# Kernel optimization log

Hardware: AMD Instinct MI355X
Metric: run time of the kernel (lower is better)

The kernel has to match this reference:

```python
import jax, jax.numpy as jnp
import numpy as np

B, S, D_IN, D_OUT = 4, 2048, 4096, 4096
QMAX = 16  # 2**bits

def setup_inputs() -> dict:
    key = jax.random.key(0)
    k1, k2, k3, k4, k5 = jax.random.split(key, 5)
    x = jax.random.normal(k1, (B, S, D_IN), dtype=jnp.float32)
    weight_q = jax.random.randint(k2, (D_OUT, D_IN), 0, QMAX, dtype=jnp.int32)
    scale = jax.random.uniform(k3, (), dtype=jnp.float32) * 0.01 + 1e-4
    zero_point = jax.random.uniform(k4, (), dtype=jnp.float32) * QMAX
    bias = jax.random.normal(k5, (D_OUT,), dtype=jnp.float32)
    return {"x": x, "weight_q": weight_q, "scale": scale,
            "zero_point": zero_point, "bias": bias}

def reference(x, weight_q, scale, zero_point, bias):
    # Dequantize: w = (q - zero_point) * scale, then y = x @ w.T + b
    w = (weight_q.astype(jnp.float32) - zero_point) * scale  # [out, in]
    return jnp.einsum('bsi,oi->bso', x, w) + bias
```

## Files before the change

### kernel.cpp

```cpp
#include <hip/hip_runtime.h>
#include <cstdint>

#define M_DIM 8192
#define N_DIM 4096
#define K_DIM 4096
#define NT    32

typedef int i32x4 __attribute__((ext_vector_type(4)));

__device__ __forceinline__ void gload_lds16(const void* g, void* l) {
  __builtin_amdgcn_global_load_lds(
      (const __attribute__((address_space(1))) unsigned int*)(uintptr_t)g,
      (__attribute__((address_space(3))) unsigned int*)(uintptr_t)l,
      16, 0, 0);
}

__global__ __launch_bounds__(256) void prep_kernel(
    const float* __restrict__ x, const int* __restrict__ q,
    signed char* __restrict__ xq, signed char* __restrict__ wq8,
    float* __restrict__ sx, float* __restrict__ si) {
  const int tid  = threadIdx.x;
  const int lane = tid & 63;
  const int wv   = tid >> 6;
  if (blockIdx.x < 2048) {
    const int row = blockIdx.x * 4 + wv;
    const float* xr = x + (size_t)row * K_DIM;
    signed char* xo = xq + (size_t)row * K_DIM;
    float4 v[16];
    float amax = 0.f;
#pragma unroll
    for (int j = 0; j < 16; ++j) {
      v[j] = *(const float4*)(xr + j * 256 + lane * 4);
      amax = fmaxf(amax, fmaxf(fmaxf(fabsf(v[j].x), fabsf(v[j].y)),
                               fmaxf(fabsf(v[j].z), fabsf(v[j].w))));
    }
#pragma unroll
    for (int off = 32; off > 0; off >>= 1)
      amax = fmaxf(amax, __shfl_xor(amax, off, 64));
    const float inv = amax > 0.f ? 127.f / amax : 0.f;
    int isum = 0;
#pragma unroll
    for (int j = 0; j < 16; ++j) {
      int ix = __float2int_rn(v[j].x * inv);
      int iy = __float2int_rn(v[j].y * inv);
      int iz = __float2int_rn(v[j].z * inv);
      int iw = __float2int_rn(v[j].w * inv);
      isum += ix + iy + iz + iw;
      char4 o; o.x = (char)ix; o.y = (char)iy; o.z = (char)iz; o.w = (char)iw;
      *(char4*)(xo + j * 256 + lane * 4) = o;
    }
#pragma unroll
    for (int off = 32; off > 0; off >>= 1)
      isum += __shfl_xor(isum, off, 64);
    if (lane == 0) {
      sx[row] = amax * (1.f / 127.f);
      si[row] = (float)isum;
    }
  } else {
    const int bid = blockIdx.x - 2048;
    const size_t total  = (size_t)N_DIM * K_DIM;
    const size_t stride = (size_t)1024 * 4096;
    for (size_t base = (size_t)bid * 4096; base < total; base += stride) {
#pragma unroll
      for (int u = 0; u < 4; ++u) {
        const size_t idx = base + (size_t)u * 1024 + tid * 4;
        int4 w = *(const int4*)(q + idx);
        char4 o; o.x = (char)w.x; o.y = (char)w.y; o.z = (char)w.z; o.w = (char)w.w;
        *(char4*)(wq8 + idx) = o;
      }
    }
  }
}

__global__ __launch_bounds__(512) void qlinear_gemm_kernel(
    const signed char* __restrict__ A,
    const signed char* __restrict__ Bm,
    const float* __restrict__ sx,
    const float* __restrict__ si,
    const float* __restrict__ scale_p, const float* __restrict__ zp_p,
    const float* __restrict__ bias,
    float* __restrict__ out) {
  __shared__ signed char sA[2][2][16384];
  __shared__ signed char sB[2][2][16384];

  const int tid  = threadIdx.x;
  const int lane = tid & 63;
  const int w    = tid >> 6;
  const int wr   = w >> 2;
  const int wc   = w & 3;
  const int lr   = lane & 15;
  const int quad = lane >> 4;

  const int bm = blockIdx.y * 256;
  const int bn = blockIdx.x * 256;

  const int srow = lane >> 3;
  const int cg   = (lane & 7) ^ srow;
  const signed char* aG = A  + (size_t)(bm + w * 8 + srow) * K_DIM + cg * 16;
  const signed char* bG = Bm + (size_t)(bn + w * 8 + srow) * K_DIM + cg * 16;
  const int dwoff = w * 1024;

#define STG_A(dst, h, c, t) \
  gload_lds16(aG + (size_t)((h) * 128 + (c) * 64) * K_DIM + (size_t)(t) * 128, \
              (dst) + (h) * 16384 + (c) * 8192 + dwoff)
#define STG_B(dst, h, c, t) \
  gload_lds16(bG + (size_t)((h) * 128 + (c) * 64) * K_DIM + (size_t)(t) * 128, \
              (dst) + (h) * 16384 + (c) * 8192 + dwoff)

  int off[2];
#pragma unroll
  for (int ks = 0; ks < 2; ++ks)
    off[ks] = lr * 128 + (((ks * 4 + quad) ^ (lr & 7)) * 16);

  i32x4 acc[8][4] = {};
  i32x4 afr[4][2];
  i32x4 bfr[2][2][2];

  {
    signed char* dA = &sA[0][0][0];
    signed char* dB = &sB[0][0][0];
    STG_B(dB, 0, 0, 0); STG_B(dB, 0, 1, 0);
    STG_B(dB, 1, 0, 0); STG_B(dB, 1, 1, 0);
    STG_A(dA, 0, 0, 0); STG_A(dA, 1, 0, 0);
    STG_A(dA, 0, 1, 0); STG_A(dA, 1, 1, 0);
  }

  for (int t = 0; t < NT; ++t) {
    const int buf = t & 1;
    const signed char* pA = &sA[buf][wr][0];
    const signed char* pB = &sB[buf][wc >> 1][0] + (wc & 1) * 8192;
    signed char* nA = &sA[buf ^ 1][0][0];
    signed char* nB = &sB[buf ^ 1][0][0];
    const bool st = (t + 1) < NT;
    const int tn = t + 1;

    asm volatile("s_waitcnt vmcnt(2)" ::: "memory");
    if (st) { STG_B(nB, 0, 0, tn); STG_B(nB, 0, 1, tn); }
    __builtin_amdgcn_s_barrier();
#pragma unroll
    for (int m = 0; m < 4; ++m)
#pragma unroll
      for (int ks = 0; ks < 2; ++ks)
        afr[m][ks] = *(const i32x4*)(pA + m * 2048 + off[ks]);
#pragma unroll
    for (int n = 0; n < 2; ++n)
#pragma unroll
      for (int ks = 0; ks < 2; ++ks)
        bfr[0][n][ks] = *(const i32x4*)(pB + n * 2048 + off[ks]);
    __builtin_amdgcn_s_setprio(1);
#pragma unroll
    for (int m = 0; m < 4; ++m)
#pragma unroll
      for (int n = 0; n < 2; ++n)
#pragma unroll
        for (int ks = 0; ks < 2; ++ks)
          acc[m][n] = __builtin_amdgcn_mfma_i32_16x16x64_i8(
              afr[m][ks], bfr[0][n][ks], acc[m][n], 0, 0, 0);
    __builtin_amdgcn_s_setprio(0);

    if (st) { STG_B(nB, 1, 0, tn); STG_B(nB, 1, 1, tn); }
    __builtin_amdgcn_s_barrier();
#pragma unroll
    for (int n = 0; n < 2; ++n)
#pragma unroll
      for (int ks = 0; ks < 2; ++ks)
        bfr[1][n][ks] = *(const i32x4*)(pB + 4096 + n * 2048 + off[ks]);
    __builtin_amdgcn_s_setprio(1);
#pragma unroll
    for (int m = 0; m < 4; ++m)
#pragma unroll
      for (int n = 0; n < 2; ++n)
#pragma unroll
        for (int ks = 0; ks < 2; ++ks)
          acc[m][2 + n] = __builtin_amdgcn_mfma_i32_16x16x64_i8(
              afr[m][ks], bfr[1][n][ks], acc[m][2 + n], 0, 0, 0);
    __builtin_amdgcn_s_setprio(0);

    if (st) asm volatile("s_waitcnt vmcnt(4)" ::: "memory");
    else    asm volatile("s_waitcnt vmcnt(0)" ::: "memory");
    if (st) { STG_A(nA, 0, 0, tn); STG_A(nA, 1, 0, tn); }
    __builtin_amdgcn_s_barrier();
#pragma unroll
    for (int m = 0; m < 4; ++m)
#pragma unroll
      for (int ks = 0; ks < 2; ++ks)
        afr[m][ks] = *(const i32x4*)(pA + 8192 + m * 2048 + off[ks]);
    __builtin_amdgcn_s_setprio(1);
#pragma unroll
    for (int m = 0; m < 4; ++m)
#pragma unroll
      for (int n = 0; n < 2; ++n)
#pragma unroll
        for (int ks = 0; ks < 2; ++ks)
          acc[4 + m][n] = __builtin_amdgcn_mfma_i32_16x16x64_i8(
              afr[m][ks], bfr[0][n][ks], acc[4 + m][n], 0, 0, 0);
    __builtin_amdgcn_s_setprio(0);

    if (st) { STG_A(nA, 0, 1, tn); STG_A(nA, 1, 1, tn); }
    __builtin_amdgcn_s_barrier();
    __builtin_amdgcn_s_setprio(1);
#pragma unroll
    for (int m = 0; m < 4; ++m)
#pragma unroll
      for (int n = 0; n < 2; ++n)
#pragma unroll
        for (int ks = 0; ks < 2; ++ks)
          acc[4 + m][2 + n] = __builtin_amdgcn_mfma_i32_16x16x64_i8(
              afr[m][ks], bfr[1][n][ks], acc[4 + m][2 + n], 0, 0, 0);
    __builtin_amdgcn_s_setprio(0);
  }
#undef STG_A
#undef STG_B

  const float scale = *scale_p;
  const float zp    = *zp_p;
#pragma unroll
  for (int i = 0; i < 8; ++i) {
    const int gm0 = bm + wr * 128 + i * 16 + quad * 4;
    float am[4], cm[4];
#pragma unroll
    for (int r = 0; r < 4; ++r) {
      am[r] = scale * sx[gm0 + r];
      cm[r] = -am[r] * zp * si[gm0 + r];
    }
#pragma unroll
    for (int j = 0; j < 4; ++j) {
      const int gn = bn + wc * 64 + j * 16 + lr;
      const float bb = bias[gn];
#pragma unroll
      for (int r = 0; r < 4; ++r)
        out[(size_t)(gm0 + r) * N_DIM + gn] =
            am[r] * (float)acc[i][j][r] + cm[r] + bb;
    }
  }
}

extern "C" void kernel_launch(void* const* d_in, const int* in_sizes, int n_in,
                              void* d_out, int out_size, void* d_ws, size_t ws_size,
                              hipStream_t stream) {
  const float* x     = (const float*)d_in[0];
  const int*   wq    = (const int*)d_in[1];
  const float* scale = (const float*)d_in[2];
  const float* zp    = (const float*)d_in[3];
  const float* bias  = (const float*)d_in[4];
  float* out = (float*)d_out;

  signed char* xq  = (signed char*)d_ws;
  signed char* wq8 = xq + (size_t)M_DIM * K_DIM;
  float* sx = (float*)(wq8 + (size_t)N_DIM * K_DIM);
  float* si = sx + M_DIM;

  prep_kernel<<<3072, 256, 0, stream>>>(x, wq, xq, wq8, sx, si);
  dim3 grid(N_DIM / 256, M_DIM / 256);
  qlinear_gemm_kernel<<<grid, 512, 0, stream>>>(xq, wq8, sx, si, scale, zp, bias, out);
}
```

Before: 385.7 us.

## Remap GEMM blocks by XCD and restructure the K-loop with fewer barriers

Launches a 1D grid and remaps block IDs so consecutive blocks on each XCD (bid&7) cover a contiguous group of output tiles, aiming for better L2 reuse of the A and B panels. The main loop drops from four barriers to two per K step: all four B loads, then all four A loads, are issued together. Fragment LDS reads are split by k-slice, with partial lgkmcnt waits so the first k-half's MFMAs can start while the second half's reads are still in flight. This raises B-fragment register use and relies on hand-placed waitcnt and sched_barrier ordering being correct.

```diff
diff --git a/kernel.cpp b/kernel.cpp
--- a/kernel.cpp
+++ b/kernel.cpp
@@ -91,8 +91,10 @@
   const int lr   = lane & 15;
   const int quad = lane >> 4;
 
-  const int bm = blockIdx.y * 256;
-  const int bn = blockIdx.x * 256;
+  const int bid = blockIdx.x;
+  const int swz = (bid & 7) * 64 + (bid >> 3);
+  const int bm  = (swz >> 4) * 256;
+  const int bn  = (swz & 15) * 256;
 
   const int srow = lane >> 3;
   const int cg   = (lane & 7) ^ srow;
@@ -114,7 +116,7 @@
 
   i32x4 acc[8][4] = {};
   i32x4 afr[4][2];
-  i32x4 bfr[2][2][2];
+  i32x4 bfr[4][2];
 
   {
     signed char* dA = &sA[0][0][0];
@@ -135,78 +137,76 @@
     const int tn = t + 1;
 
     asm volatile("s_waitcnt vmcnt(2)" ::: "memory");
-    if (st) { STG_B(nB, 0, 0, tn); STG_B(nB, 0, 1, tn); }
     __builtin_amdgcn_s_barrier();
-#pragma unroll
-    for (int m = 0; m < 4; ++m)
-#pragma unroll
-      for (int ks = 0; ks < 2; ++ks)
-        afr[m][ks] = *(const i32x4*)(pA + m * 2048 + off[ks]);
-#pragma unroll
-    for (int n = 0; n < 2; ++n)
-#pragma unroll
-      for (int ks = 0; ks < 2; ++ks)
-        bfr[0][n][ks] = *(const i32x4*)(pB + n * 2048 + off[ks]);
-    __builtin_amdgcn_s_setprio(1);
-#pragma unroll
-    for (int m = 0; m < 4; ++m)
-#pragma unroll
-      for (int n = 0; n < 2; ++n)
-#pragma unroll
-        for (int ks = 0; ks < 2; ++ks)
-          acc[m][n] = __builtin_amdgcn_mfma_i32_16x16x64_i8(
-              afr[m][ks], bfr[0][n][ks], acc[m][n], 0, 0, 0);
-    __builtin_amdgcn_s_setprio(0);
-
-    if (st) { STG_B(nB, 1, 0, tn); STG_B(nB, 1, 1, tn); }
-    __builtin_amdgcn_s_barrier();
-#pragma unroll
-    for (int n = 0; n < 2; ++n)
-#pragma unroll
-      for (int ks = 0; ks < 2; ++ks)
-        bfr[1][n][ks] = *(const i32x4*)(pB + 4096 + n * 2048 + off[ks]);
-    __builtin_amdgcn_s_setprio(1);
-#pragma unroll
-    for (int m = 0; m < 4; ++m)
-#pragma unroll
-      for (int n = 0; n < 2; ++n)
-#pragma unroll
-        for (int ks = 0; ks < 2; ++ks)
-          acc[m][2 + n] = __builtin_amdgcn_mfma_i32_16x16x64_i8(
-              afr[m][ks], bfr[1][n][ks], acc[m][2 + n], 0, 0, 0);
+    if (st) { STG_B(nB, 0, 0, tn); STG_B(nB, 0, 1, tn);
+              STG_B(nB, 1, 0, tn); STG_B(nB, 1, 1, tn); }
+#pragma unroll
+    for (int m = 0; m < 4; ++m)
+      afr[m][0] = *(const i32x4*)(pA + m * 2048 + off[0]);
+#pragma unroll
+    for (int n = 0; n < 4; ++n)
+      bfr[n][0] = *(const i32x4*)(pB + n * 2048 + off[0]);
+    __builtin_amdgcn_sched_barrier(0);
+#pragma unroll
+    for (int m = 0; m < 4; ++m)
+      afr[m][1] = *(const i32x4*)(pA + m * 2048 + off[1]);
+#pragma unroll
+    for (int n = 0; n < 4; ++n)
+      bfr[n][1] = *(const i32x4*)(pB + n * 2048 + off[1]);
+    __builtin_amdgcn_sched_barrier(0);
+    asm volatile("s_waitcnt lgkmcnt(8)" ::: "memory");
+    __builtin_amdgcn_sched_barrier(0);
+    __builtin_amdgcn_s_setprio(1);
+#pragma unroll
+    for (int m = 0; m < 4; ++m)
+#pragma unroll
+      for (int n = 0; n < 4; ++n)
+        acc[m][n] = __builtin_amdgcn_mfma_i32_16x16x64_i8(
+            afr[m][0], bfr[n][0], acc[m][n], 0, 0, 0);
+    __builtin_amdgcn_s_setprio(0);
+    asm volatile("s_waitcnt lgkmcnt(0)" ::: "memory");
+    __builtin_amdgcn_sched_barrier(0);
+    __builtin_amdgcn_s_setprio(1);
+#pragma unroll
+    for (int m = 0; m < 4; ++m)
+#pragma unroll
+      for (int n = 0; n < 4; ++n)
+        acc[m][n] = __builtin_amdgcn_mfma_i32_16x16x64_i8(
+            afr[m][1], bfr[n][1], acc[m][n], 0, 0, 0);
     __builtin_amdgcn_s_setprio(0);
 
     if (st) asm volatile("s_waitcnt vmcnt(4)" ::: "memory");
     else    asm volatile("s_waitcnt vmcnt(0)" ::: "memory");
-    if (st) { STG_A(nA, 0, 0, tn); STG_A(nA, 1, 0, tn); }
     __builtin_amdgcn_s_barrier();
-#pragma unroll
-    for (int m = 0; m < 4; ++m)
-#pragma unroll
-      for (int ks = 0; ks < 2; ++ks)
-        afr[m][ks] = *(const i32x4*)(pA + 8192 + m * 2048 + off[ks]);
-    __builtin_amdgcn_s_setprio(1);
-#pragma unroll
-    for (int m = 0; m < 4; ++m)
-#pragma unroll
-      for (int n = 0; n < 2; ++n)
-#pragma unroll
-        for (int ks = 0; ks < 2; ++ks)
-          acc[4 + m][n] = __builtin_amdgcn_mfma_i32_16x16x64_i8(
-              afr[m][ks], bfr[0][n][ks], acc[4 + m][n], 0, 0, 0);
-    __builtin_amdgcn_s_setprio(0);
-
-    if (st) { STG_A(nA, 0, 1, tn); STG_A(nA, 1, 1, tn); }
-    __builtin_amdgcn_s_barrier();
-    __builtin_amdgcn_s_setprio(1);
-#pragma unroll
-    for (int m = 0; m < 4; ++m)
-#pragma unroll
-      for (int n = 0; n < 2; ++n)
-#pragma unroll
-        for (int ks = 0; ks < 2; ++ks)
-          acc[4 + m][2 + n] = __builtin_amdgcn_mfma_i32_16x16x64_i8(
-              afr[m][ks], bfr[1][n][ks], acc[4 + m][2 + n], 0, 0, 0);
+    if (st) { STG_A(nA, 0, 0, tn); STG_A(nA, 1, 0, tn);
+              STG_A(nA, 0, 1, tn); STG_A(nA, 1, 1, tn); }
+#pragma unroll
+    for (int m = 0; m < 4; ++m)
+      afr[m][0] = *(const i32x4*)(pA + 8192 + m * 2048 + off[0]);
+    __builtin_amdgcn_sched_barrier(0);
+#pragma unroll
+    for (int m = 0; m < 4; ++m)
+      afr[m][1] = *(const i32x4*)(pA + 8192 + m * 2048 + off[1]);
+    __builtin_amdgcn_sched_barrier(0);
+    asm volatile("s_waitcnt lgkmcnt(4)" ::: "memory");
+    __builtin_amdgcn_sched_barrier(0);
+    __builtin_amdgcn_s_setprio(1);
+#pragma unroll
+    for (int m = 0; m < 4; ++m)
+#pragma unroll
+      for (int n = 0; n < 4; ++n)
+        acc[4 + m][n] = __builtin_amdgcn_mfma_i32_16x16x64_i8(
+            afr[m][0], bfr[n][0], acc[4 + m][n], 0, 0, 0);
+    __builtin_amdgcn_s_setprio(0);
+    asm volatile("s_waitcnt lgkmcnt(0)" ::: "memory");
+    __builtin_amdgcn_sched_barrier(0);
+    __builtin_amdgcn_s_setprio(1);
+#pragma unroll
+    for (int m = 0; m < 4; ++m)
+#pragma unroll
+      for (int n = 0; n < 4; ++n)
+        acc[4 + m][n] = __builtin_amdgcn_mfma_i32_16x16x64_i8(
+            afr[m][1], bfr[n][1], acc[4 + m][n], 0, 0, 0);
     __builtin_amdgcn_s_setprio(0);
   }
 #undef STG_A
@@ -251,6 +251,5 @@
   float* si = sx + M_DIM;
 
   prep_kernel<<<3072, 256, 0, stream>>>(x, wq, xq, wq8, sx, si);
-  dim3 grid(N_DIM / 256, M_DIM / 256);
-  qlinear_gemm_kernel<<<grid, 512, 0, stream>>>(xq, wq8, sx, si, scale, zp, bias, out);
-}
+  qlinear_gemm_kernel<<<512, 512, 0, stream>>>(xq, wq8, sx, si, scale, zp, bias, out);
+}
```

Measured after the change: 385.5 us. Within noise of the previous version (-0.0%).

## Switch GEMM to 32x32x32 int8 MFMA and add XCD-aware block swizzle

Applied to the files above, without the earlier changes.

Replaces the 16x16x64 int8 MFMA tiles with 32x32x32 int8 MFMA. This changes the LDS fragment offsets, the accumulator layout (i32x16) and the epilogue row/column mapping. The aim is fewer MFMA instructions and fewer LDS reads per unit of compute. The 2D grid also becomes a 1D grid with a swizzle that spreads neighbouring tiles across the 8 XCDs, which should improve L2 reuse. The risks are more register pressure from 16-wide accumulators and a scattered epilogue store pattern.

```diff
diff --git a/kernel.cpp b/kernel.cpp
--- a/kernel.cpp
+++ b/kernel.cpp
@@ -6,7 +6,8 @@
 #define K_DIM 4096
 #define NT    32
 
-typedef int i32x4 __attribute__((ext_vector_type(4)));
+typedef int i32x4  __attribute__((ext_vector_type(4)));
+typedef int i32x16 __attribute__((ext_vector_type(16)));
 
 __device__ __forceinline__ void gload_lds16(const void* g, void* l) {
   __builtin_amdgcn_global_load_lds(
@@ -88,11 +89,11 @@
   const int w    = tid >> 6;
   const int wr   = w >> 2;
   const int wc   = w & 3;
-  const int lr   = lane & 15;
-  const int quad = lane >> 4;
-
-  const int bm = blockIdx.y * 256;
-  const int bn = blockIdx.x * 256;
+
+  const int bid = blockIdx.x;
+  const int swz = (bid & 7) * 64 + (bid >> 3);
+  const int bm  = (swz >> 4) * 256;
+  const int bn  = (swz & 15) * 256;
 
   const int srow = lane >> 3;
   const int cg   = (lane & 7) ^ srow;
@@ -107,14 +108,12 @@
   gload_lds16(bG + (size_t)((h) * 128 + (c) * 64) * K_DIM + (size_t)(t) * 128, \
               (dst) + (h) * 16384 + (c) * 8192 + dwoff)
 
-  int off[2];
-#pragma unroll
-  for (int ks = 0; ks < 2; ++ks)
-    off[ks] = lr * 128 + (((ks * 4 + quad) ^ (lr & 7)) * 16);
-
-  i32x4 acc[8][4] = {};
-  i32x4 afr[4][2];
-  i32x4 bfr[2][2][2];
+  int loff[4];
+#pragma unroll
+  for (int ks = 0; ks < 4; ++ks)
+    loff[ks] = (lane & 31) * 128 + (((ks * 2 + (lane >> 5)) ^ (lane & 7)) * 16);
+
+  i32x16 acc[4][2] = {};
 
   {
     signed char* dA = &sA[0][0][0];
@@ -134,46 +133,40 @@
     const bool st = (t + 1) < NT;
     const int tn = t + 1;
 
+    i32x4 afr[2][4], afr2[2][4], bfr0[4], bfr1[4];
+
     asm volatile("s_waitcnt vmcnt(2)" ::: "memory");
     if (st) { STG_B(nB, 0, 0, tn); STG_B(nB, 0, 1, tn); }
     __builtin_amdgcn_s_barrier();
 #pragma unroll
-    for (int m = 0; m < 4; ++m)
-#pragma unroll
-      for (int ks = 0; ks < 2; ++ks)
-        afr[m][ks] = *(const i32x4*)(pA + m * 2048 + off[ks]);
-#pragma unroll
-    for (int n = 0; n < 2; ++n)
-#pragma unroll
-      for (int ks = 0; ks < 2; ++ks)
-        bfr[0][n][ks] = *(const i32x4*)(pB + n * 2048 + off[ks]);
-    __builtin_amdgcn_s_setprio(1);
-#pragma unroll
-    for (int m = 0; m < 4; ++m)
-#pragma unroll
-      for (int n = 0; n < 2; ++n)
-#pragma unroll
-        for (int ks = 0; ks < 2; ++ks)
-          acc[m][n] = __builtin_amdgcn_mfma_i32_16x16x64_i8(
-              afr[m][ks], bfr[0][n][ks], acc[m][n], 0, 0, 0);
+    for (int m = 0; m < 2; ++m)
+#pragma unroll
+      for (int ks = 0; ks < 4; ++ks)
+        afr[m][ks] = *(const i32x4*)(pA + m * 4096 + loff[ks]);
+#pragma unroll
+    for (int ks = 0; ks < 4; ++ks)
+      bfr0[ks] = *(const i32x4*)(pB + loff[ks]);
+    __builtin_amdgcn_s_setprio(1);
+#pragma unroll
+    for (int m = 0; m < 2; ++m)
+#pragma unroll
+      for (int ks = 0; ks < 4; ++ks)
+        acc[m][0] = __builtin_amdgcn_mfma_i32_32x32x32_i8(
+            afr[m][ks], bfr0[ks], acc[m][0], 0, 0, 0);
     __builtin_amdgcn_s_setprio(0);
 
     if (st) { STG_B(nB, 1, 0, tn); STG_B(nB, 1, 1, tn); }
     __builtin_amdgcn_s_barrier();
 #pragma unroll
-    for (int n = 0; n < 2; ++n)
-#pragma unroll
-      for (int ks = 0; ks < 2; ++ks)
-        bfr[1][n][ks] = *(const i32x4*)(pB + 4096 + n * 2048 + off[ks]);
-    __builtin_amdgcn_s_setprio(1);
-#pragma unroll
-    for (int m = 0; m < 4; ++m)
-#pragma unroll
-      for (int n = 0; n < 2; ++n)
-#pragma unroll
-        for (int ks = 0; ks < 2; ++ks)
-          acc[m][2 + n] = __builtin_amdgcn_mfma_i32_16x16x64_i8(
-              afr[m][ks], bfr[1][n][ks], acc[m][2 + n], 0, 0, 0);
+    for (int ks = 0; ks < 4; ++ks)
+      bfr1[ks] = *(const i32x4*)(pB + 4096 + loff[ks]);
+    __builtin_amdgcn_s_setprio(1);
+#pragma unroll
+    for (int m = 0; m < 2; ++m)
+#pragma unroll
+      for (int ks = 0; ks < 4; ++ks)
+        acc[m][1] = __builtin_amdgcn_mfma_i32_32x32x32_i8(
+            afr[m][ks], bfr1[ks], acc[m][1], 0, 0, 0);
     __builtin_amdgcn_s_setprio(0);
 
     if (st) asm volatile("s_waitcnt vmcnt(4)" ::: "memory");
@@ -181,32 +174,28 @@
     if (st) { STG_A(nA, 0, 0, tn); STG_A(nA, 1, 0, tn); }
     __builtin_amdgcn_s_barrier();
 #pragma unroll
-    for (int m = 0; m < 4; ++m)
-#pragma unroll
-      for (int ks = 0; ks < 2; ++ks)
-        afr[m][ks] = *(const i32x4*)(pA + 8192 + m * 2048 + off[ks]);
-    __builtin_amdgcn_s_setprio(1);
-#pragma unroll
-    for (int m = 0; m < 4; ++m)
-#pragma unroll
-      for (int n = 0; n < 2; ++n)
-#pragma unroll
-        for (int ks = 0; ks < 2; ++ks)
-          acc[4 + m][n] = __builtin_amdgcn_mfma_i32_16x16x64_i8(
-              afr[m][ks], bfr[0][n][ks], acc[4 + m][n], 0, 0, 0);
+    for (int m = 0; m < 2; ++m)
+#pragma unroll
+      for (int ks = 0; ks < 4; ++ks)
+        afr2[m][ks] = *(const i32x4*)(pA + 8192 + m * 4096 + loff[ks]);
+    __builtin_amdgcn_s_setprio(1);
+#pragma unroll
+    for (int m = 0; m < 2; ++m)
+#pragma unroll
+      for (int ks = 0; ks < 4; ++ks)
+        acc[2 + m][0] = __builtin_amdgcn_mfma_i32_32x32x32_i8(
+            afr2[m][ks], bfr0[ks], acc[2 + m][0], 0, 0, 0);
     __builtin_amdgcn_s_setprio(0);
 
     if (st) { STG_A(nA, 0, 1, tn); STG_A(nA, 1, 1, tn); }
     __builtin_amdgcn_s_barrier();
     __builtin_amdgcn_s_setprio(1);
 #pragma unroll
-    for (int m = 0; m < 4; ++m)
-#pragma unroll
-      for (int n = 0; n < 2; ++n)
-#pragma unroll
-        for (int ks = 0; ks < 2; ++ks)
-          acc[4 + m][2 + n] = __builtin_amdgcn_mfma_i32_16x16x64_i8(
-              afr[m][ks], bfr[1][n][ks], acc[4 + m][2 + n], 0, 0, 0);
+    for (int m = 0; m < 2; ++m)
+#pragma unroll
+      for (int ks = 0; ks < 4; ++ks)
+        acc[2 + m][1] = __builtin_amdgcn_mfma_i32_32x32x32_i8(
+            afr2[m][ks], bfr1[ks], acc[2 + m][1], 0, 0, 0);
     __builtin_amdgcn_s_setprio(0);
   }
 #undef STG_A
@@ -215,22 +204,25 @@
   const float scale = *scale_p;
   const float zp    = *zp_p;
 #pragma unroll
-  for (int i = 0; i < 8; ++i) {
-    const int gm0 = bm + wr * 128 + i * 16 + quad * 4;
-    float am[4], cm[4];
-#pragma unroll
-    for (int r = 0; r < 4; ++r) {
-      am[r] = scale * sx[gm0 + r];
-      cm[r] = -am[r] * zp * si[gm0 + r];
-    }
-#pragma unroll
-    for (int j = 0; j < 4; ++j) {
-      const int gn = bn + wc * 64 + j * 16 + lr;
+  for (int m = 0; m < 4; ++m) {
+    const int rbase = bm + wr * 128 + m * 32 + 4 * (lane >> 5);
+    float am[16], cm[16];
+#pragma unroll
+    for (int r = 0; r < 16; ++r) {
+      const int row = rbase + (r & 3) + 8 * (r >> 2);
+      am[r] = scale * sx[row];
+      cm[r] = -am[r] * zp * si[row];
+    }
+#pragma unroll
+    for (int n = 0; n < 2; ++n) {
+      const int gn = bn + wc * 64 + n * 32 + (lane & 31);
       const float bb = bias[gn];
 #pragma unroll
-      for (int r = 0; r < 4; ++r)
-        out[(size_t)(gm0 + r) * N_DIM + gn] =
-            am[r] * (float)acc[i][j][r] + cm[r] + bb;
+      for (int r = 0; r < 16; ++r) {
+        const int row = rbase + (r & 3) + 8 * (r >> 2);
+        out[(size_t)row * N_DIM + gn] =
+            am[r] * (float)acc[m][n][r] + cm[r] + bb;
+      }
     }
   }
 }
@@ -251,6 +243,5 @@
   float* si = sx + M_DIM;
 
   prep_kernel<<<3072, 256, 0, stream>>>(x, wq, xq, wq8, sx, si);
-  dim3 grid(N_DIM / 256, M_DIM / 256);
-  qlinear_gemm_kernel<<<grid, 512, 0, stream>>>(xq, wq8, sx, si, scale, zp, bias, out);
-}
+  qlinear_gemm_kernel<<<512, 512, 0, stream>>>(xq, wq8, sx, si, scale, zp, bias, out);
+}
```

New measurement: 397.8 us. 1.03x slower.

## Shrink int8 GEMM block tile from 256x256 to 128x128 with 4 waves

Applied to the files above, without the earlier changes.

Changes the int8 MFMA GEMM from 256x256 tiles with 8 waves per block to 128x128 tiles with 4 waves, and restructures the LDS staging, wave mapping and accumulator layout to match. The result is a 2048-block grid instead of 512 and 64KB of LDS per block instead of 128KB, so more blocks fit on each CU and the CUs are filled better. The cost is lower operand reuse per tile, which roughly doubles global/L2 traffic for A and B relative to the MFMA work.

```diff
diff --git a/kernel.cpp b/kernel.cpp
--- a/kernel.cpp
+++ b/kernel.cpp
@@ -72,7 +72,7 @@
   }
 }
 
-__global__ __launch_bounds__(512) void qlinear_gemm_kernel(
+__global__ __launch_bounds__(256) void qlinear_gemm_kernel(
     const signed char* __restrict__ A,
     const signed char* __restrict__ Bm,
     const float* __restrict__ sx,
@@ -80,19 +80,19 @@
     const float* __restrict__ scale_p, const float* __restrict__ zp_p,
     const float* __restrict__ bias,
     float* __restrict__ out) {
-  __shared__ signed char sA[2][2][16384];
-  __shared__ signed char sB[2][2][16384];
+  __shared__ signed char sA[2][16384];
+  __shared__ signed char sB[2][16384];
 
   const int tid  = threadIdx.x;
   const int lane = tid & 63;
   const int w    = tid >> 6;
-  const int wr   = w >> 2;
-  const int wc   = w & 3;
+  const int wr   = w >> 1;
+  const int wc   = w & 1;
   const int lr   = lane & 15;
   const int quad = lane >> 4;
 
-  const int bm = blockIdx.y * 256;
-  const int bn = blockIdx.x * 256;
+  const int bm = blockIdx.y * 128;
+  const int bn = blockIdx.x * 128;
 
   const int srow = lane >> 3;
   const int cg   = (lane & 7) ^ srow;
@@ -100,45 +100,44 @@
   const signed char* bG = Bm + (size_t)(bn + w * 8 + srow) * K_DIM + cg * 16;
   const int dwoff = w * 1024;
 
-#define STG_A(dst, h, c, t) \
-  gload_lds16(aG + (size_t)((h) * 128 + (c) * 64) * K_DIM + (size_t)(t) * 128, \
-              (dst) + (h) * 16384 + (c) * 8192 + dwoff)
-#define STG_B(dst, h, c, t) \
-  gload_lds16(bG + (size_t)((h) * 128 + (c) * 64) * K_DIM + (size_t)(t) * 128, \
-              (dst) + (h) * 16384 + (c) * 8192 + dwoff)
+#define STG_A(dst, c, t) \
+  gload_lds16(aG + (size_t)((c) * 32) * K_DIM + (size_t)(t) * 128, \
+              (dst) + (c) * 4096 + dwoff)
+#define STG_B(dst, c, t) \
+  gload_lds16(bG + (size_t)((c) * 32) * K_DIM + (size_t)(t) * 128, \
+              (dst) + (c) * 4096 + dwoff)
 
   int off[2];
 #pragma unroll
   for (int ks = 0; ks < 2; ++ks)
     off[ks] = lr * 128 + (((ks * 4 + quad) ^ (lr & 7)) * 16);
 
-  i32x4 acc[8][4] = {};
-  i32x4 afr[4][2];
-  i32x4 bfr[2][2][2];
+  i32x4 acc[4][4] = {};
 
   {
-    signed char* dA = &sA[0][0][0];
-    signed char* dB = &sB[0][0][0];
-    STG_B(dB, 0, 0, 0); STG_B(dB, 0, 1, 0);
-    STG_B(dB, 1, 0, 0); STG_B(dB, 1, 1, 0);
-    STG_A(dA, 0, 0, 0); STG_A(dA, 1, 0, 0);
-    STG_A(dA, 0, 1, 0); STG_A(dA, 1, 1, 0);
+    signed char* dA = &sA[0][0];
+    signed char* dB = &sB[0][0];
+    STG_B(dB, 0, 0); STG_B(dB, 1, 0); STG_B(dB, 2, 0); STG_B(dB, 3, 0);
+    STG_A(dA, 0, 0); STG_A(dA, 2, 0);
+    STG_A(dA, 1, 0); STG_A(dA, 3, 0);
   }
 
   for (int t = 0; t < NT; ++t) {
     const int buf = t & 1;
-    const signed char* pA = &sA[buf][wr][0];
-    const signed char* pB = &sB[buf][wc >> 1][0] + (wc & 1) * 8192;
-    signed char* nA = &sA[buf ^ 1][0][0];
-    signed char* nB = &sB[buf ^ 1][0][0];
+    const signed char* pA = &sA[buf][0] + wr * 8192;
+    const signed char* pB = &sB[buf][0] + wc * 8192;
+    signed char* nA = &sA[buf ^ 1][0];
+    signed char* nB = &sB[buf ^ 1][0];
     const bool st = (t + 1) < NT;
     const int tn = t + 1;
 
+    i32x4 afr[2][2], afr2[2][2], bfr0[2][2], bfr1[2][2];
+
     asm volatile("s_waitcnt vmcnt(2)" ::: "memory");
-    if (st) { STG_B(nB, 0, 0, tn); STG_B(nB, 0, 1, tn); }
-    __builtin_amdgcn_s_barrier();
-#pragma unroll
-    for (int m = 0; m < 4; ++m)
+    if (st) { STG_B(nB, 0, tn); STG_B(nB, 1, tn); }
+    __builtin_amdgcn_s_barrier();
+#pragma unroll
+    for (int m = 0; m < 2; ++m)
 #pragma unroll
       for (int ks = 0; ks < 2; ++ks)
         afr[m][ks] = *(const i32x4*)(pA + m * 2048 + off[ks]);
@@ -146,67 +145,67 @@
     for (int n = 0; n < 2; ++n)
 #pragma unroll
       for (int ks = 0; ks < 2; ++ks)
-        bfr[0][n][ks] = *(const i32x4*)(pB + n * 2048 + off[ks]);
-    __builtin_amdgcn_s_setprio(1);
-#pragma unroll
-    for (int m = 0; m < 4; ++m)
+        bfr0[n][ks] = *(const i32x4*)(pB + n * 2048 + off[ks]);
+    __builtin_amdgcn_s_setprio(1);
+#pragma unroll
+    for (int m = 0; m < 2; ++m)
 #pragma unroll
       for (int n = 0; n < 2; ++n)
 #pragma unroll
         for (int ks = 0; ks < 2; ++ks)
           acc[m][n] = __builtin_amdgcn_mfma_i32_16x16x64_i8(
-              afr[m][ks], bfr[0][n][ks], acc[m][n], 0, 0, 0);
-    __builtin_amdgcn_s_setprio(0);
-
-    if (st) { STG_B(nB, 1, 0, tn); STG_B(nB, 1, 1, tn); }
+              afr[m][ks], bfr0[n][ks], acc[m][n], 0, 0, 0);
+    __builtin_amdgcn_s_setprio(0);
+
+    if (st) { STG_B(nB, 2, tn); STG_B(nB, 3, tn); }
     __builtin_amdgcn_s_barrier();
 #pragma unroll
     for (int n = 0; n < 2; ++n)
 #pragma unroll
       for (int ks = 0; ks < 2; ++ks)
-        bfr[1][n][ks] = *(const i32x4*)(pB + 4096 + n * 2048 + off[ks]);
-    __builtin_amdgcn_s_setprio(1);
-#pragma unroll
-    for (int m = 0; m < 4; ++m)
+        bfr1[n][ks] = *(const i32x4*)(pB + 4096 + n * 2048 + off[ks]);
+    __builtin_amdgcn_s_setprio(1);
+#pragma unroll
+    for (int m = 0; m < 2; ++m)
 #pragma unroll
       for (int n = 0; n < 2; ++n)
 #pragma unroll
         for (int ks = 0; ks < 2; ++ks)
           acc[m][2 + n] = __builtin_amdgcn_mfma_i32_16x16x64_i8(
-              afr[m][ks], bfr[1][n][ks], acc[m][2 + n], 0, 0, 0);
+              afr[m][ks], bfr1[n][ks], acc[m][2 + n], 0, 0, 0);
     __builtin_amdgcn_s_setprio(0);
 
     if (st) asm volatile("s_waitcnt vmcnt(4)" ::: "memory");
     else    asm volatile("s_waitcnt vmcnt(0)" ::: "memory");
-    if (st) { STG_A(nA, 0, 0, tn); STG_A(nA, 1, 0, tn); }
-    __builtin_amdgcn_s_barrier();
-#pragma unroll
-    for (int m = 0; m < 4; ++m)
-#pragma unroll
-      for (int ks = 0; ks < 2; ++ks)
-        afr[m][ks] = *(const i32x4*)(pA + 8192 + m * 2048 + off[ks]);
-    __builtin_amdgcn_s_setprio(1);
-#pragma unroll
-    for (int m = 0; m < 4; ++m)
-#pragma unroll
-      for (int n = 0; n < 2; ++n)
-#pragma unroll
-        for (int ks = 0; ks < 2; ++ks)
-          acc[4 + m][n] = __builtin_amdgcn_mfma_i32_16x16x64_i8(
-              afr[m][ks], bfr[0][n][ks], acc[4 + m][n], 0, 0, 0);
-    __builtin_amdgcn_s_setprio(0);
-
-    if (st) { STG_A(nA, 0, 1, tn); STG_A(nA, 1, 1, tn); }
-    __builtin_amdgcn_s_barrier();
-    __builtin_amdgcn_s_setprio(1);
-#pragma unroll
-    for (int m = 0; m < 4; ++m)
-#pragma unroll
-      for (int n = 0; n < 2; ++n)
-#pragma unroll
-        for (int ks = 0; ks < 2; ++ks)
-          acc[4 + m][2 + n] = __builtin_amdgcn_mfma_i32_16x16x64_i8(
-              afr[m][ks], bfr[1][n][ks], acc[4 + m][2 + n], 0, 0, 0);
+    if (st) { STG_A(nA, 0, tn); STG_A(nA, 2, tn); }
+    __builtin_amdgcn_s_barrier();
+#pragma unroll
+    for (int m = 0; m < 2; ++m)
+#pragma unroll
+      for (int ks = 0; ks < 2; ++ks)
+        afr2[m][ks] = *(const i32x4*)(pA + 4096 + m * 2048 + off[ks]);
+    __builtin_amdgcn_s_setprio(1);
+#pragma unroll
+    for (int m = 0; m < 2; ++m)
+#pragma unroll
+      for (int n = 0; n < 2; ++n)
+#pragma unroll
+        for (int ks = 0; ks < 2; ++ks)
+          acc[2 + m][n] = __builtin_amdgcn_mfma_i32_16x16x64_i8(
+              afr2[m][ks], bfr0[n][ks], acc[2 + m][n], 0, 0, 0);
+    __builtin_amdgcn_s_setprio(0);
+
+    if (st) { STG_A(nA, 1, tn); STG_A(nA, 3, tn); }
+    __builtin_amdgcn_s_barrier();
+    __builtin_amdgcn_s_setprio(1);
+#pragma unroll
+    for (int m = 0; m < 2; ++m)
+#pragma unroll
+      for (int n = 0; n < 2; ++n)
+#pragma unroll
+        for (int ks = 0; ks < 2; ++ks)
+          acc[2 + m][2 + n] = __builtin_amdgcn_mfma_i32_16x16x64_i8(
+              afr2[m][ks], bfr1[n][ks], acc[2 + m][2 + n], 0, 0, 0);
     __builtin_amdgcn_s_setprio(0);
   }
 #undef STG_A
@@ -215,8 +214,8 @@
   const float scale = *scale_p;
   const float zp    = *zp_p;
 #pragma unroll
-  for (int i = 0; i < 8; ++i) {
-    const int gm0 = bm + wr * 128 + i * 16 + quad * 4;
+  for (int i = 0; i < 4; ++i) {
+    const int gm0 = bm + wr * 64 + i * 16 + quad * 4;
     float am[4], cm[4];
 #pragma unroll
     for (int r = 0; r < 4; ++r) {
@@ -251,6 +250,6 @@
   float* si = sx + M_DIM;
 
   prep_kernel<<<3072, 256, 0, stream>>>(x, wq, xq, wq8, sx, si);
-  dim3 grid(N_DIM / 256, M_DIM / 256);
-  qlinear_gemm_kernel<<<grid, 512, 0, stream>>>(xq, wq8, sx, si, scale, zp, bias, out);
-}
+  dim3 grid(N_DIM / 128, M_DIM / 128);
+  qlinear_gemm_kernel<<<grid, 256, 0, stream>>>(xq, wq8, sx, si, scale, zp, bias, out);
+}
```

New measurement: 407.4 us. +5.6%, slower.
